# Optimization experiments

Hardware: AMD Instinct MI355X
Metric: run time of the kernel (lower is better)

Reference implementation:

```python
import jax, jax.numpy as jnp
import numpy as np

DIM = 256
HEADS = 8
HEAD_DIM = DIM // HEADS
SCALE = HEAD_DIM ** -0.5
WD, WH, WW = 2, 7, 7
N = WD * WH * WW            # 98 tokens per window
NW = 256                    # windows per sample
B = 2048                    # batch * num_windows
PBT_LEN = (2 * WD - 1) * (2 * WH - 1) * (2 * WW - 1)  # 507


def _relative_position_index():
    # Deterministic buffer from __init__: [N, N] int indices into pbt rows.
    coords = np.stack(np.meshgrid(np.arange(WD), np.arange(WH), np.arange(WW), indexing='ij'))
    coords = coords.reshape(3, -1)                      # [3, N]
    rel = coords[:, :, None] - coords[:, None, :]       # [3, N, N]
    rel = rel.transpose(1, 2, 0).copy()                 # [N, N, 3]
    rel[..., 0] += WD - 1
    rel[..., 1] += WH - 1
    rel[..., 2] += WW - 1
    rel[..., 0] *= (2 * WH - 1) * (2 * WW - 1)
    rel[..., 1] *= 2 * WW - 1
    return rel.sum(-1)                                  # [N, N]


def setup_inputs() -> dict:
    key = jax.random.key(0)
    ks = jax.random.split(key, 6)
    x = jax.random.normal(ks[0], (B, N, DIM), dtype=jnp.float32)
    mask = jax.random.normal(ks[1], (NW, N, N), dtype=jnp.float32)
    pbt = jax.random.normal(ks[2], (PBT_LEN, HEADS), dtype=jnp.float32) * 0.02
    qkv_w = jax.random.normal(ks[3], (3 * DIM, DIM), dtype=jnp.float32) * 0.02
    proj_w = jax.random.normal(ks[4], (DIM, DIM), dtype=jnp.float32) * 0.02
    proj_b = jax.random.normal(ks[5], (DIM,), dtype=jnp.float32) * 0.02
    rpi = jnp.asarray(_relative_position_index(), dtype=jnp.int32)
    return {"x": x, "mask": mask, "pbt": pbt, "qkv_w": qkv_w,
            "proj_w": proj_w, "proj_b": proj_b, "rpi": rpi}


def reference(x, mask, pbt, qkv_w, proj_w, proj_b, rpi):
    b, n, c = x.shape
    qkv = x @ qkv_w.T                                   # [b, n, 3c] (qkv_bias=False)
    q, k, v = jnp.split(qkv, 3, axis=-1)
    to_heads = lambda t: t.reshape(b, n, HEADS, HEAD_DIM).transpose(0, 2, 1, 3)
    q, k, v = to_heads(q), to_heads(k), to_heads(v)     # [b, h, n, d]

    attn = SCALE * jnp.einsum('bhnd,bhmd->bhnm', q, k)  # [b, h, n, n]
    # gathered relative-position bias: pbt[rpi] -> [n, n, h] -> [h, n, n]
    bias = pbt[rpi.reshape(-1)].reshape(n, n, HEADS).transpose(2, 0, 1)
    attn = attn + bias[None]

    n_w = mask.shape[0]
    attn = attn.reshape(b // n_w, n_w, HEADS, n, n) + mask[None, :, None]
    attn = attn.reshape(b, HEADS, n, n)

    attn = jax.nn.softmax(attn, axis=-1)
    out = jnp.einsum('bhnm,bhmd->bhnd', attn, v)        # [b, h, n, d]
    out = out.transpose(0, 2, 1, 3).reshape(b, n, c)
    return out @ proj_w.T + proj_b
```

## Files before the change

### kernel.cpp

```cpp
#include <hip/hip_runtime.h>
#include <hip/hip_bf16.h>
#include <math.h>

typedef float f32x4 __attribute__((ext_vector_type(4)));
typedef __bf16 bf16x8 __attribute__((ext_vector_type(8)));

#define NTOK 98
#define NWIN 2048
#define NN (NTOK * NTOK)
#define SCALE 0.17677669529663689f
#define MROWS (NWIN * NTOK)
#define PSTRIDE 9408

__device__ __forceinline__ void g2l16(const void* g, void* l) {
  typedef __attribute__((address_space(1))) const unsigned int GU;
  typedef __attribute__((address_space(3))) unsigned int LU;
  __builtin_amdgcn_global_load_lds((GU*)g, (LU*)l, 16, 0, 0);
}

__global__ void prep_kernel(const float* __restrict__ qkv_w, const float* __restrict__ proj_w,
                            const float* __restrict__ pbt, const int* __restrict__ rpi,
                            const float* __restrict__ mask,
                            __bf16* __restrict__ qkvw_b, __bf16* __restrict__ projw_b,
                            float* __restrict__ cmb) {
  int i = blockIdx.x * 256 + threadIdx.x;
  if (i < 768 * 256) qkvw_b[i] = (__bf16)qkv_w[i];
  if (i < 256 * 256) projw_b[i] = (__bf16)proj_w[i];
  if (i < 256 * 8 * NTOK * 128) {
    int mh = i / (NTOK * 128);
    int rem = i - mh * (NTOK * 128);
    int row = rem >> 7, j = rem & 127;
    if (j < NTOK) {
      int m = mh >> 3, h = mh & 7;
      cmb[i] = pbt[rpi[row * NTOK + j] * 8 + h] + mask[m * NN + row * NTOK + j];
    } else {
      cmb[i] = 0.f;
    }
  }
}

__launch_bounds__(256)
__global__ void gemm_qkv(const float* __restrict__ A, const __bf16* __restrict__ W,
                         __bf16* __restrict__ C) {
  __shared__ __align__(16) char As[128 * 512];
  __shared__ __align__(16) char Bs[128 * 128];
  const int m0 = blockIdx.x * 128;
  const int tid = threadIdx.x;
  const int lane = tid & 63;
  const int wid = tid >> 6;
  const int wm = wid & 1, wn = wid >> 1;
  const int lr = lane & 15;
  const int lg = lane >> 4;

  for (int c = tid; c < 128 * 32; c += 256) {
    int row = c >> 5, slot = c & 31;
    const float* ap = A + (size_t)(m0 + row) * 256 + slot * 8;
    float4 f0 = *(const float4*)ap;
    float4 f1 = *(const float4*)(ap + 4);
    bf16x8 hv;
    hv[0] = (__bf16)f0.x; hv[1] = (__bf16)f0.y; hv[2] = (__bf16)f0.z; hv[3] = (__bf16)f0.w;
    hv[4] = (__bf16)f1.x; hv[5] = (__bf16)f1.y; hv[6] = (__bf16)f1.z; hv[7] = (__bf16)f1.w;
    *(bf16x8*)(As + row * 512 + ((slot * 16) ^ ((row & 7) << 4))) = hv;
  }
  __syncthreads();

  for (int nt = 0; nt < 6; ++nt) {
    const int n0 = nt * 128;
    f32x4 acc[4][4] = {};
    for (int k0 = 0; k0 < 256; k0 += 64) {
#pragma unroll
      for (int it = 0; it < 4; ++it) {
        int c = wid * 4 + it;
        int row = c * 8 + (lane >> 3);
        int src_chunk = (lane & 7) ^ (row & 7);
        g2l16(W + (size_t)(n0 + row) * 256 + k0 + src_chunk * 8, (void*)(Bs + c * 1024));
      }
      __syncthreads();
#pragma unroll
      for (int kk = 0; kk < 2; ++kk) {
        bf16x8 a[4], b[4];
#pragma unroll
        for (int m = 0; m < 4; ++m) {
          int row = wm * 64 + m * 16 + lr;
          a[m] = *(const bf16x8*)(As + row * 512 +
                                  ((k0 * 2 + kk * 64 + lg * 16) ^ ((row & 7) << 4)));
        }
#pragma unroll
        for (int n = 0; n < 4; ++n) {
          int row = wn * 64 + n * 16 + lr;
          b[n] = *(const bf16x8*)(Bs + row * 128 + ((kk * 64 + lg * 16) ^ ((row & 7) << 4)));
        }
#pragma unroll
        for (int m = 0; m < 4; ++m)
#pragma unroll
          for (int n = 0; n < 4; ++n)
            acc[m][n] = __builtin_amdgcn_mfma_f32_16x16x32_bf16(a[m], b[n], acc[m][n], 0, 0, 0);
      }
      __syncthreads();
    }
#pragma unroll
    for (int m = 0; m < 4; ++m)
#pragma unroll
      for (int r = 0; r < 4; ++r) {
        unsigned row = m0 + wm * 64 + m * 16 + lg * 4 + r;
        unsigned win = row / NTOK;
        unsigned tok = row - win * NTOK;
#pragma unroll
        for (int n = 0; n < 4; ++n) {
          int col = n0 + wn * 64 + n * 16 + lr;
          int sec = col >> 8, dd = col & 255;
          int h = dd >> 5, d = dd & 31;
          C[(size_t)(win * 8 + h) * PSTRIDE + (size_t)sec * 3136 + tok * 32 + d] =
              (__bf16)acc[m][n][r];
        }
      }
  }
}

__launch_bounds__(128)
__global__ void attn_kernel(const __bf16* __restrict__ qkv, const float* __restrict__ cmb,
                            __bf16* __restrict__ y) {
  __shared__ __align__(16) char VTB[8192];
  int bx = blockIdx.x;
  int lb = (bx & 7) * 2048 + (bx >> 3);
  const int win = lb >> 3, h = lb & 7;
  const int tid = threadIdx.x;
  const int lane = tid & 63, wv = tid >> 6;
  const int lr = lane & 15, lg = lane >> 4;
  const f32x4 fz = {0.f, 0.f, 0.f, 0.f};

  const __bf16* qw = qkv + (size_t)(win * 8 + h) * PSTRIDE;
  const __bf16* kw = qw + 3136;
  const __bf16* vw = qw + 6272;
  const float* cw = cmb + (size_t)((win & 255) * 8 + h) * (NTOK * 128);

  for (int c = tid; c < 512; c += 128) {
    int j = c & 127; int jc = j < NTOK ? j : NTOK - 1;
    int d8 = (c >> 7) << 3;
    bf16x8 vv = *(const bf16x8*)(vw + jc * 32 + d8);
#pragma unroll
    for (int e = 0; e < 8; ++e) {
      int d = d8 + e;
      *(__bf16*)(VTB + d * 256 + ((2 * j) ^ ((d & 7) << 4))) = vv[e];
    }
  }

  bf16x8 bk[7];
#pragma unroll
  for (int jt = 0; jt < 7; ++jt) {
    int brow = ((jt >> 1) << 5) + ((lr >> 2) << 3) + ((jt & 1) << 2) + (lr & 3);
    int browc = brow < NTOK ? brow : NTOK - 1;
    bk[jt] = *(const bf16x8*)(kw + browc * 32 + lg * 8);
  }
  __syncthreads();

  for (int it = wv; it < 7; it += 2) {
    const int i0 = it * 16;
    const int qrow = i0 + lr;
    const int qrowc = qrow < NTOK ? qrow : NTOK - 1;
    bf16x8 aq = *(const bf16x8*)(qw + qrowc * 32 + lg * 8);

    const float* cr = cw + qrowc * 128;
    float4 cv[7];
#pragma unroll
    for (int jt = 0; jt < 7; ++jt) {
      int kb = ((jt >> 1) << 5) + lg * 8 + ((jt & 1) << 2);
      cv[jt] = *(const float4*)(cr + kb);
    }

    f32x4 s[7];
#pragma unroll
    for (int jt = 0; jt < 7; ++jt)
      s[jt] = __builtin_amdgcn_mfma_f32_16x16x32_bf16(bk[jt], aq, fz, 0, 0, 0);

    float sv[7][4];
    float mx = -INFINITY;
#pragma unroll
    for (int jt = 0; jt < 7; ++jt) {
      int kb = ((jt >> 1) << 5) + lg * 8 + ((jt & 1) << 2);
#pragma unroll
      for (int r = 0; r < 4; ++r) {
        float xv = (kb + r < NTOK) ? fmaf(SCALE, s[jt][r], (&cv[jt].x)[r]) : -INFINITY;
        sv[jt][r] = xv;
        mx = fmaxf(mx, xv);
      }
    }
    mx = fmaxf(mx, __shfl_xor(mx, 16));
    mx = fmaxf(mx, __shfl_xor(mx, 32));
    float sum = 0.f;
#pragma unroll
    for (int jt = 0; jt < 7; ++jt)
#pragma unroll
      for (int r = 0; r < 4; ++r) {
        float p = __expf(sv[jt][r] - mx);
        sv[jt][r] = p;
        sum += p;
      }
    sum += __shfl_xor(sum, 16);
    sum += __shfl_xor(sum, 32);
    const float rinv = 1.f / sum;

    bf16x8 pa[4];
#pragma unroll
    for (int ks = 0; ks < 4; ++ks)
#pragma unroll
      for (int e = 0; e < 8; ++e) {
        int jt = 2 * ks + (e >> 2);
        pa[ks][e] = (jt < 7) ? (__bf16)sv[jt][e & 3] : (__bf16)0.f;
      }

    float rv[4];
#pragma unroll
    for (int r = 0; r < 4; ++r) rv[r] = __shfl(rinv, lg * 4 + r);

#pragma unroll
    for (int dt = 0; dt < 2; ++dt) {
      f32x4 o = fz;
#pragma unroll
      for (int ks = 0; ks < 4; ++ks) {
        int vrow = dt * 16 + lr;
        bf16x8 vb = *(const bf16x8*)(VTB + vrow * 256 + ((ks * 64 + lg * 16) ^ ((vrow & 7) << 4)));
        o = __builtin_amdgcn_mfma_f32_16x16x32_bf16(pa[ks], vb, o, 0, 0, 0);
      }
#pragma unroll
      for (int r = 0; r < 4; ++r) {
        int row = i0 + lg * 4 + r;
        if (row < NTOK)
          y[((size_t)win * NTOK + row) * 256 + h * 32 + dt * 16 + lr] = (__bf16)(o[r] * rv[r]);
      }
    }
  }
}

__launch_bounds__(256)
__global__ void gemm_proj(const __bf16* __restrict__ A, const __bf16* __restrict__ W,
                          const float* __restrict__ pb, float* __restrict__ C) {
  __shared__ __align__(16) char As[128 * 128];
  __shared__ __align__(16) char Bs[128 * 128];
  const int bid = blockIdx.x;
  const int m0 = (bid / 2) * 128;
  const int n0 = (bid % 2) * 128;
  const int tid = threadIdx.x;
  const int lane = tid & 63;
  const int wid = tid >> 6;
  const int wm = wid & 1, wn = wid >> 1;
  const int lr = lane & 15;
  const int lg = lane >> 4;
  f32x4 acc[4][4] = {};

  for (int k0 = 0; k0 < 256; k0 += 64) {
#pragma unroll
    for (int it = 0; it < 4; ++it) {
      int c = wid * 4 + it;
      int row = c * 8 + (lane >> 3);
      int src_chunk = (lane & 7) ^ (row & 7);
      g2l16(A + (size_t)(m0 + row) * 256 + k0 + src_chunk * 8, (void*)(As + c * 1024));
      g2l16(W + (size_t)(n0 + row) * 256 + k0 + src_chunk * 8, (void*)(Bs + c * 1024));
    }
    __syncthreads();
#pragma unroll
    for (int kk = 0; kk < 2; ++kk) {
      bf16x8 a[4], b[4];
#pragma unroll
      for (int m = 0; m < 4; ++m) {
        int row = wm * 64 + m * 16 + lr;
        a[m] = *(const bf16x8*)(As + row * 128 + ((kk * 64 + lg * 16) ^ ((row & 7) << 4)));
      }
#pragma unroll
      for (int n = 0; n < 4; ++n) {
        int row = wn * 64 + n * 16 + lr;
        b[n] = *(const bf16x8*)(Bs + row * 128 + ((kk * 64 + lg * 16) ^ ((row & 7) << 4)));
      }
#pragma unroll
      for (int m = 0; m < 4; ++m)
#pragma unroll
        for (int n = 0; n < 4; ++n)
          acc[m][n] = __builtin_amdgcn_mfma_f32_16x16x32_bf16(a[m], b[n], acc[m][n], 0, 0, 0);
    }
    __syncthreads();
  }
#pragma unroll
  for (int m = 0; m < 4; ++m) {
    int row = m0 + wm * 64 + m * 16 + lg * 4;
#pragma unroll
    for (int n = 0; n < 4; ++n) {
      int col = n0 + wn * 64 + n * 16 + lr;
      float bv = pb[col];
#pragma unroll
      for (int r = 0; r < 4; ++r)
        C[(size_t)(row + r) * 256 + col] = acc[m][n][r] + bv;
    }
  }
}

extern "C" void kernel_launch(void* const* d_in, const int* in_sizes, int n_in,
                              void* d_out, int out_size, void* d_ws, size_t ws_size,
                              hipStream_t stream) {
  const float* x      = (const float*)d_in[0];
  const float* mask   = (const float*)d_in[1];
  const float* pbt    = (const float*)d_in[2];
  const float* qkv_w  = (const float*)d_in[3];
  const float* proj_w = (const float*)d_in[4];
  const float* proj_b = (const float*)d_in[5];
  const int*   rpi    = (const int*)d_in[6];
  float* out = (float*)d_out;

  char* ws = (char*)d_ws;
  __bf16* qkv      = (__bf16*)(ws);
  __bf16* y        = (__bf16*)(ws + 308281344);
  __bf16* qkvw_b   = (__bf16*)(ws + 411041792);
  __bf16* projw_b  = (__bf16*)(ws + 411435008);
  float*  cmb      = (float*) (ws + 411566080);

  int prep_n = 256 * 8 * NTOK * 128;
  prep_kernel<<<(prep_n + 255) / 256, 256, 0, stream>>>(qkv_w, proj_w, pbt, rpi, mask,
                                                        qkvw_b, projw_b, cmb);
  gemm_qkv<<<MROWS / 128, 256, 0, stream>>>(x, qkvw_b, qkv);
  attn_kernel<<<NWIN * 8, 128, 0, stream>>>(qkv, cmb, y);
  gemm_proj<<<(MROWS / 128) * 2, 256, 0, stream>>>(y, projw_b, proj_b, out);
}
```

Measured before the change: 510.7 us.

## Double-buffer weight tiles in QKV GEMM with 32-wide K steps

Splits the QKV GEMM weight staging into two 8 KB LDS buffers with 32-element K slices and prefetches the next slice via global_load_lds while MFMAs run on the current one. This replaces the load-sync-compute-sync pattern with a single barrier per K step, aiming to hide global load latency. It needs a new swizzle for 64-byte rows and doubles the number of K iterations, and the prefetch is not waited on explicitly beyond the barrier.

After: 509.5 us. About the same (-0.2%).

```diff
diff --git a/kernel.cpp b/kernel.cpp
--- a/kernel.cpp
+++ b/kernel.cpp
@@ -42,8 +42,8 @@
 __launch_bounds__(256)
 __global__ void gemm_qkv(const float* __restrict__ A, const __bf16* __restrict__ W,
                          __bf16* __restrict__ C) {
-  __shared__ __align__(16) char As[128 * 512];
-  __shared__ __align__(16) char Bs[128 * 128];
+  __shared__ __align__(16) char As[65536];
+  __shared__ __align__(16) char Bs[2][8192];
   const int m0 = blockIdx.x * 128;
   const int tid = threadIdx.x;
   const int lane = tid & 63;
@@ -67,37 +67,50 @@
   for (int nt = 0; nt < 6; ++nt) {
     const int n0 = nt * 128;
     f32x4 acc[4][4] = {};
-    for (int k0 = 0; k0 < 256; k0 += 64) {
-#pragma unroll
-      for (int it = 0; it < 4; ++it) {
-        int c = wid * 4 + it;
-        int row = c * 8 + (lane >> 3);
-        int src_chunk = (lane & 7) ^ (row & 7);
-        g2l16(W + (size_t)(n0 + row) * 256 + k0 + src_chunk * 8, (void*)(Bs + c * 1024));
-      }
+
+#pragma unroll
+    for (int it2 = 0; it2 < 2; ++it2) {
+      int wc = wid * 2 + it2;
+      int cc = wc * 64 + lane;
+      int row = cc >> 2, slot = cc & 3;
+      int sw = (row & 3) ^ ((row >> 3) & 3);
+      g2l16(W + (size_t)(n0 + row) * 256 + ((slot ^ sw) * 8), (void*)(Bs[0] + wc * 1024));
+    }
+    __syncthreads();
+
+    for (int ks = 0; ks < 8; ++ks) {
+      const int cur = ks & 1;
+      if (ks < 7) {
+#pragma unroll
+        for (int it2 = 0; it2 < 2; ++it2) {
+          int wc = wid * 2 + it2;
+          int cc = wc * 64 + lane;
+          int row = cc >> 2, slot = cc & 3;
+          int sw = (row & 3) ^ ((row >> 3) & 3);
+          g2l16(W + (size_t)(n0 + row) * 256 + (ks + 1) * 32 + ((slot ^ sw) * 8),
+                (void*)(Bs[cur ^ 1] + wc * 1024));
+        }
+      }
+      bf16x8 a[4], b[4];
+#pragma unroll
+      for (int m = 0; m < 4; ++m) {
+        int row = wm * 64 + m * 16 + lr;
+        a[m] = *(const bf16x8*)(As + row * 512 + ((ks * 64 + lg * 16) ^ ((row & 7) << 4)));
+      }
+#pragma unroll
+      for (int n = 0; n < 4; ++n) {
+        int row = wn * 64 + n * 16 + lr;
+        int sw = (row & 3) ^ ((row >> 3) & 3);
+        b[n] = *(const bf16x8*)(Bs[cur] + row * 64 + ((lg * 16) ^ (sw << 4)));
+      }
+#pragma unroll
+      for (int m = 0; m < 4; ++m)
+#pragma unroll
+        for (int n = 0; n < 4; ++n)
+          acc[m][n] = __builtin_amdgcn_mfma_f32_16x16x32_bf16(a[m], b[n], acc[m][n], 0, 0, 0);
       __syncthreads();
-#pragma unroll
-      for (int kk = 0; kk < 2; ++kk) {
-        bf16x8 a[4], b[4];
-#pragma unroll
-        for (int m = 0; m < 4; ++m) {
-          int row = wm * 64 + m * 16 + lr;
-          a[m] = *(const bf16x8*)(As + row * 512 +
-                                  ((k0 * 2 + kk * 64 + lg * 16) ^ ((row & 7) << 4)));
-        }
-#pragma unroll
-        for (int n = 0; n < 4; ++n) {
-          int row = wn * 64 + n * 16 + lr;
-          b[n] = *(const bf16x8*)(Bs + row * 128 + ((kk * 64 + lg * 16) ^ ((row & 7) << 4)));
-        }
-#pragma unroll
-        for (int m = 0; m < 4; ++m)
-#pragma unroll
-          for (int n = 0; n < 4; ++n)
-            acc[m][n] = __builtin_amdgcn_mfma_f32_16x16x32_bf16(a[m], b[n], acc[m][n], 0, 0, 0);
-      }
-      __syncthreads();
-    }
+    }
+
 #pragma unroll
     for (int m = 0; m < 4; ++m)
 #pragma unroll
```
